# Optimization experiments

Measured on AMD Instinct MI355X. Metric: run time of the kernel, lower is better.

The kernel has to match this reference:

```python
import jax, jax.numpy as jnp
import numpy as np

VOCAB = 32000
D_MODEL = 768
D_FF = 3072
N_LAYERS = 12
SEQ = 2048
BATCH = 8
EPS = 1e-5  # torch LayerNorm default


def _layernorm(x, g, b):
    mu = jnp.mean(x, axis=-1, keepdims=True)
    var = jnp.mean(jnp.square(x - mu), axis=-1, keepdims=True)
    return (x - mu) * jax.lax.rsqrt(var + EPS) * g + b


def setup_inputs() -> dict:
    key = jax.random.key(0)
    ks = jax.random.split(key, 12)
    tokens = jax.random.randint(ks[0], (BATCH, SEQ), 0, VOCAB)
    embed = jax.random.normal(ks[1], (VOCAB, D_MODEL), dtype=jnp.float32) * 0.02
    ln1_g = jnp.ones((N_LAYERS, D_MODEL), dtype=jnp.float32)
    ln1_b = jnp.zeros((N_LAYERS, D_MODEL), dtype=jnp.float32)
    ln2_g = jnp.ones((N_LAYERS, D_MODEL), dtype=jnp.float32)
    ln2_b = jnp.zeros((N_LAYERS, D_MODEL), dtype=jnp.float32)
    W1 = jax.random.normal(ks[2], (N_LAYERS, D_MODEL, D_FF), dtype=jnp.float32) * (1.0 / np.sqrt(D_MODEL))
    b1 = jnp.zeros((N_LAYERS, D_FF), dtype=jnp.float32)
    W2 = jax.random.normal(ks[3], (N_LAYERS, D_FF, D_MODEL), dtype=jnp.float32) * (1.0 / np.sqrt(D_FF))
    b2 = jnp.zeros((N_LAYERS, D_MODEL), dtype=jnp.float32)
    Wout = jax.random.normal(ks[4], (D_MODEL, VOCAB), dtype=jnp.float32) * (1.0 / np.sqrt(D_MODEL))
    bout = jnp.zeros((VOCAB,), dtype=jnp.float32)
    return {"tokens": tokens, "embed": embed, "ln1_g": ln1_g, "ln1_b": ln1_b,
            "ln2_g": ln2_g, "ln2_b": ln2_b, "W1": W1, "b1": b1, "W2": W2, "b2": b2,
            "Wout": Wout, "bout": bout}


def reference(tokens, embed, ln1_g, ln1_b, ln2_g, ln2_b, W1, b1, W2, b2, Wout, bout):
    # embedding lookup; embed_size == d_model so projection is Identity.
    x = embed[tokens]  # [B, S, D]
    # dropout is inference-mode identity
    for l in range(N_LAYERS):
        res = x
        h = _layernorm(x, ln1_g[l], ln1_b[l])
        h = jnp.fft.fft2(h, axes=(-2, -1)).real  # token mixing, keep real part
        x = h + res
        res = x
        h = _layernorm(x, ln2_g[l], ln2_b[l])
        h = jax.nn.gelu(jnp.einsum('bsd,df->bsf', h, W1[l]) + b1[l], approximate=False)
        h = jnp.einsum('bsf,fd->bsd', h, W2[l]) + b2[l]
        x = h + res
    # predict from last position
    return jnp.einsum('bd,dv->bv', x[:, -1, :], Wout) + bout
```

## Files before the change

kernel.cpp:

```cpp
#include <hip/hip_runtime.h>
#include <hip/hip_bf16.h>

typedef unsigned short u16;
typedef unsigned long long u64;
typedef __attribute__((ext_vector_type(8))) __bf16 bf16x8;
typedef __attribute__((ext_vector_type(4))) float f32x4;
typedef __attribute__((ext_vector_type(4))) unsigned short u16x4;

#define BB 8
#define SS 2048
#define DD 768
#define DFF 3072
#define NL 12
#define ROWS (BB*SS)
#define VOC 32000

__device__ __forceinline__ u16 f2bf(float f){
  union { float f; unsigned u; } v; v.f = f;
  unsigned u = v.u;
  u += 0x7FFF + ((u >> 16) & 1);
  return (u16)(u >> 16);
}
__device__ __forceinline__ float bf2f(u16 b){
  union { unsigned u; float f; } v; v.u = ((unsigned)b) << 16; return v.f;
}

__global__ void k_embed(const int* __restrict__ tok, const float4* __restrict__ emb,
                        float4* __restrict__ x){
  int i = blockIdx.x*256 + threadIdx.x;
  if (i >= ROWS*192) return;
  int row = i/192, c = i - row*192;
  x[i] = emb[(long)tok[row]*192 + c];
}

__global__ void k_dftD(u16* __restrict__ out){
  int i = blockIdx.x*256 + threadIdx.x;
  if (i >= 1536*768) return;
  int n = i/768, k = i - n*768;
  int nn = (n < 768) ? n : n - 768;
  int m = (nn*k) % 768;
  float a = 2.0f*(float)m/768.0f;
  out[i] = f2bf((n < 768) ? cospif(a) : sinpif(a));
}

__global__ void k_dftS2(u16* __restrict__ out){
  int i = blockIdx.x*256 + threadIdx.x;
  if (i >= 2048*2048) return;
  int t = i >> 11, slot = i & 2047;
  int ss = (slot <= 1024) ? slot : slot - 1024;
  int m = (t*ss) & 2047;
  float a = (float)m * (1.0f/1024.0f);
  out[i] = f2bf((slot <= 1024) ? cospif(a) : -sinpif(a));
}

template<bool RES>
__global__ void k_ln1_fold(float* __restrict__ x, const u16* __restrict__ t4,
                           const float* __restrict__ bias,
                           const float* __restrict__ g, const float* __restrict__ b,
                           u16* __restrict__ hp, u16* __restrict__ hm){
  int gid = blockIdx.x*4 + (threadIdx.x >> 6);
  if (gid >= 8*1025) return;
  int bb = gid/1025, t = gid - bb*1025;
  int u = (2048 - t) & 2047;
  long rt = (long)bb*2048 + t, ru = (long)bb*2048 + u;
  int lane = threadIdx.x & 63;
  float vt[12], vu[12];
  #pragma unroll
  for (int j = 0; j < 12; j++){
    int e = lane + j*64;
    float a0 = x[rt*DD + e], a1 = x[ru*DD + e];
    if (RES){
      float bv = bias[e];
      a0 += bf2f(t4[rt*DD + e]) + bv;
      a1 += bf2f(t4[ru*DD + e]) + bv;
    }
    vt[j] = a0; vu[j] = a1;
  }
  float s0 = 0.f, s1 = 0.f;
  #pragma unroll
  for (int j = 0; j < 12; j++){ s0 += vt[j]; s1 += vu[j]; }
  #pragma unroll
  for (int o = 32; o > 0; o >>= 1){ s0 += __shfl_xor(s0, o); s1 += __shfl_xor(s1, o); }
  float mu0 = s0*(1.0f/768.0f), mu1 = s1*(1.0f/768.0f);
  float q0 = 0.f, q1 = 0.f;
  #pragma unroll
  for (int j = 0; j < 12; j++){ float d0 = vt[j]-mu0, d1 = vu[j]-mu1; q0 += d0*d0; q1 += d1*d1; }
  #pragma unroll
  for (int o = 32; o > 0; o >>= 1){ q0 += __shfl_xor(q0, o); q1 += __shfl_xor(q1, o); }
  float r0 = rsqrtf(q0*(1.0f/768.0f) + 1e-5f);
  float r1 = rsqrtf(q1*(1.0f/768.0f) + 1e-5f);
  const bool single = (t == 0) || (t == 1024);
  u16* hpr = hp + ((long)bb*1280 + t)*DD;
  u16* hmr = hm + ((long)bb*1024 + t)*DD;
  #pragma unroll
  for (int j = 0; j < 12; j++){
    int e = lane + j*64;
    if (RES){ x[rt*DD + e] = vt[j]; x[ru*DD + e] = vu[j]; }
    float ht = (vt[j]-mu0)*r0*g[e] + b[e];
    float hu = (vu[j]-mu1)*r1*g[e] + b[e];
    hpr[e] = f2bf(single ? ht : ht + hu);
    if (!single) hmr[e] = f2bf(ht - hu);
  }
}

__global__ void k_ln2_fuse(float* __restrict__ x, const u16* __restrict__ t2,
                           const float* __restrict__ g, const float* __restrict__ b,
                           u16* __restrict__ h, int rmul, int radd, int nrows){
  int gid = blockIdx.x*4 + (threadIdx.x >> 6);
  if (gid >= nrows) return;
  long row = (long)gid*rmul + radd;
  int lane = threadIdx.x & 63;
  float v[12];
  float s = 0.f;
  #pragma unroll
  for (int j = 0; j < 12; j++){
    int e = lane + j*64;
    long ix = row*DD + e;
    float a = x[ix] + bf2f(t2[ix]);
    v[j] = a; s += a;
  }
  #pragma unroll
  for (int o = 32; o > 0; o >>= 1) s += __shfl_xor(s, o);
  float mu = s * (1.0f/768.0f);
  float q = 0.f;
  #pragma unroll
  for (int j = 0; j < 12; j++){ float d = v[j]-mu; q += d*d; }
  #pragma unroll
  for (int o = 32; o > 0; o >>= 1) q += __shfl_xor(q, o);
  float rs = rsqrtf(q * (1.0f/768.0f) + 1e-5f);
  #pragma unroll
  for (int j = 0; j < 12; j++){
    int e = lane + j*64;
    x[row*DD + e] = v[j];
    h[row*DD + e] = f2bf((v[j]-mu)*rs*g[e] + b[e]);
  }
}

__global__ void k_transpose_cvt(const float* __restrict__ src, u16* __restrict__ dst,
                                int R, int C){
  __shared__ float t[32][33];
  int bx = blockIdx.x*32, by = blockIdx.y*32;
  int tx = threadIdx.x, ty = threadIdx.y;
  #pragma unroll
  for (int i = 0; i < 4; i++) t[ty+i*8][tx] = src[(long)(by+ty+i*8)*C + bx+tx];
  __syncthreads();
  #pragma unroll
  for (int i = 0; i < 4; i++) dst[(long)(bx+ty+i*8)*R + by+tx] = f2bf(t[tx][ty+i*8]);
}

#define EPI_ADDX 1
#define EPI_GELU 2
#define EPI_OUTB 3

#define MFMA_Q(H, G, BF) do { \
  __builtin_amdgcn_s_setprio(1); \
  _Pragma("unroll") \
  for (int mm = 0; mm < 4; ++mm) \
    _Pragma("unroll") \
    for (int nn = 0; nn < 2; ++nn) \
      _Pragma("unroll") \
      for (int ks2 = 0; ks2 < 2; ++ks2) \
        acc[((H)<<2)+mm][((G)<<1)+nn] = __builtin_amdgcn_mfma_f32_16x16x32_bf16( \
            aF[mm][ks2], BF[nn][ks2], acc[((H)<<2)+mm][((G)<<1)+nn], 0, 0, 0); \
  __builtin_amdgcn_s_setprio(0); \
} while(0)

#define GEMM_CORE_BODY \
  f32x4 acc[8][4] = {}; \
  bf16x8 aF[4][2], b0F[2][2], b1F[2][2]; \
  auto stage = [&](int tile){ \
    if (tile >= NT) return; \
    _Pragma("unroll") \
    for (int hh = 0; hh < 4; ++hh){ \
      const int isB   = ((hh + 1) >> 1) & 1; \
      const int rhalf = ((hh >> 1) & 1) << 7; \
      const u16* src = isB ? Bb : Ab; \
      const int rb = (isB ? bn : bm) + rhalf + sRow; \
      const u16* s0 = src + (long)rb * K + (tile << 6) + sCol; \
      u16* d0 = &lds[tile & 1][isB][rhalf + (wave << 3)][0]; \
      __builtin_amdgcn_global_load_lds((__attribute__((address_space(1))) void*)(s0), \
                                       (__attribute__((address_space(3))) void*)(d0), 16, 0, 0); \
      __builtin_amdgcn_global_load_lds((__attribute__((address_space(1))) void*)(s0 + ((long)K << 6)), \
                                       (__attribute__((address_space(3))) void*)(d0 + 64*64), 16, 0, 0); \
    } \
  }; \
  auto readA = [&](int c, int H){ \
    const u16* base = &lds[c][0][(H << 7) + (wm << 6)][0]; \
    _Pragma("unroll") \
    for (int mm = 0; mm < 4; ++mm) \
      _Pragma("unroll") \
      for (int ks2 = 0; ks2 < 2; ++ks2) \
        aF[mm][ks2] = *(const bf16x8*)&base[((mm<<4) + fr)*64 + (((ks2<<5) + fks8) ^ swz)]; \
  }; \
  auto readB = [&](int c, int G, bf16x8 (&bF)[2][2]){ \
    const u16* base = &lds[c][1][(G << 7) + (wn << 5)][0]; \
    _Pragma("unroll") \
    for (int nn = 0; nn < 2; ++nn) \
      _Pragma("unroll") \
      for (int ks2 = 0; ks2 < 2; ++ks2) \
        bF[nn][ks2] = *(const bf16x8*)&base[((nn<<4) + fr)*64 + (((ks2<<5) + fks8) ^ swz)]; \
  }; \
  stage(0); \
  __syncthreads(); \
  for (int T = 0; T < NT; ++T){ \
    stage(T + 1); \
    int c = T & 1; \
    readA(c, 0); readB(c, 0, b0F); \
    MFMA_Q(0, 0, b0F); \
    readB(c, 1, b1F); \
    MFMA_Q(0, 1, b1F); \
    readA(c, 1); \
    MFMA_Q(1, 1, b1F); \
    MFMA_Q(1, 0, b0F); \
    __syncthreads(); \
  }

template<int EPI>
__global__ __launch_bounds__(512, 2)
void k_gemm256(const u16* __restrict__ A, const u16* __restrict__ BT,
               int Nt, int N, int K, int NT, long aBS, long btBS, int rowOffPerZ,
               int mMul, int mAdd,
               float* __restrict__ X, const float* __restrict__ bias,
               u16* __restrict__ OUT){
  __shared__ __align__(16) u16 lds[2][2][256][64];
  const int tid  = threadIdx.x;
  const int wave = tid >> 6, lane = tid & 63;
  const int wm = wave >> 2, wn = wave & 3;

  const int bz = blockIdx.z;
  const u16* Ab = A + (long)bz*aBS;
  const u16* Bb = BT + (long)bz*btBS;
  const int rowOff = bz*rowOffPerZ;

  const int nwg = gridDim.x;
  const int id  = blockIdx.x;
  const int sw  = ((nwg & 7) == 0) ? ((id & 7) * (nwg >> 3) + (id >> 3)) : id;
  const int bn = (sw % Nt) << 8;
  const int bm = ((sw / Nt) * mMul + mAdd) << 8;

  const int fr   = lane & 15;
  const int fks8 = (lane >> 4) << 3;
  const int swz  = (fr & 7) << 3;
  const int sRow = (wave << 3) + (lane >> 3);
  const int sCol = ((lane & 7) ^ ((lane >> 3) & 7)) << 3;

  GEMM_CORE_BODY

  const int er = (lane >> 4) << 2, ec = lane & 15;
  #pragma unroll
  for (int mi = 0; mi < 8; ++mi){
    int row = bm + ((mi >> 2) << 7) + (wm << 6) + ((mi & 3) << 4) + er;
    #pragma unroll
    for (int ni = 0; ni < 4; ++ni){
      int col = bn + ((ni >> 1) << 7) + (wn << 5) + ((ni & 1) << 4) + ec;
      f32x4 v = acc[mi][ni];
      if constexpr (EPI == EPI_ADDX){
        float bv = bias ? bias[col] : 0.0f;
        #pragma unroll
        for (int r = 0; r < 4; r++)
          X[(long)(rowOff + row + r)*N + col] += v[r] + bv;
      } else if constexpr (EPI == EPI_OUTB){
        #pragma unroll
        for (int r = 0; r < 4; r++)
          OUT[(long)(rowOff + row + r)*N + col] = f2bf(v[r]);
      } else {
        float bv = bias[col];
        #pragma unroll
        for (int r = 0; r < 4; r++){
          float tt = v[r] + bv;
          OUT[(long)(row + r)*N + col] = f2bf(0.5f*tt*(1.0f + erff(tt*0.70710678118654752f)));
        }
      }
    }
  }
}

__global__ __launch_bounds__(512, 2)
void k_gemm1(const u16* __restrict__ hp, const u16* __restrict__ hm,
             const u16* __restrict__ dftD, u16* __restrict__ Ff){
  __shared__ __align__(16) u16 lds[2][2][256][64];
  const int tid  = threadIdx.x;
  const int wave = tid >> 6, lane = tid & 63;
  const int wm = wave >> 2, wn = wave & 3;

  const int K = 768, NT = 12;
  const int nwg = gridDim.x;
  const int id  = blockIdx.x;
  int sw  = (id & 7) * (nwg >> 3) + (id >> 3);
  const bool plus = (sw < 120);
  const u16* Ab;
  const u16* Bb;
  if (plus){ Ab = hp; Bb = dftD; }
  else     { sw -= 120; Ab = hm; Bb = dftD + 768*768; }
  const int bn = (sw % 3) << 8;
  const int bm = (sw / 3) << 8;

  const int fr   = lane & 15;
  const int fks8 = (lane >> 4) << 3;
  const int swz  = (fr & 7) << 3;
  const int sRow = (wave << 3) + (lane >> 3);
  const int sCol = ((lane & 7) ^ ((lane >> 3) & 7)) << 3;

  GEMM_CORE_BODY

  const int er = (lane >> 4) << 2, ec = lane & 15;
  #pragma unroll
  for (int mi = 0; mi < 8; ++mi){
    int row = bm + ((mi >> 2) << 7) + (wm << 6) + ((mi & 3) << 4) + er;
    #pragma unroll
    for (int ni = 0; ni < 4; ++ni){
      int col = bn + ((ni >> 1) << 7) + (wn << 5) + ((ni & 1) << 4) + ec;
      f32x4 v = acc[mi][ni];
      u16x4 pk;
      #pragma unroll
      for (int r = 0; r < 4; r++) pk[r] = f2bf(v[r]);
      if (plus){
        int b = row / 1280, t = row - b*1280;
        u16* dst = Ff + ((long)(b*768 + col))*2048 + t;
        if (t <= 1020)      *(u16x4*)dst = pk;
        else if (t == 1024) dst[0] = pk[0];
      } else {
        int b = row >> 10, t = row & 1023;
        u16* dst = Ff + ((long)(b*768 + col))*2048 + 1024 + t;
        if (t == 0){ dst[1] = pk[1]; dst[2] = pk[2]; dst[3] = pk[3]; }
        else        *(u16x4*)dst = pk;
      }
    }
  }
}

__global__ void k_logits(const float* __restrict__ x, const float* __restrict__ Wout,
                         const float* __restrict__ bout, float* __restrict__ out){
  __shared__ float xl[8][768];
  int tid = threadIdx.x;
  for (int i = tid; i < 8*768; i += 256){
    int b = i/768, d = i - b*768;
    xl[b][d] = x[((long)(b*2048 + 2047))*768 + d];
  }
  __syncthreads();
  int v = blockIdx.x*256 + tid;
  float acc[8];
  float bv = bout[v];
  #pragma unroll
  for (int b = 0; b < 8; b++) acc[b] = bv;
  for (int d = 0; d < 768; d++){
    float w = Wout[(long)d*VOC + v];
    #pragma unroll
    for (int b = 0; b < 8; b++) acc[b] += xl[b][d]*w;
  }
  #pragma unroll
  for (int b = 0; b < 8; b++) out[(long)b*VOC + v] = acc[b];
}

extern "C" void kernel_launch(void* const* d_in, const int* in_sizes, int n_in,
                              void* d_out, int out_size, void* d_ws, size_t ws_size,
                              hipStream_t stream){
  const int*   tokens = (const int*)d_in[0];
  const float* embed  = (const float*)d_in[1];
  const float* ln1_g  = (const float*)d_in[2];
  const float* ln1_b  = (const float*)d_in[3];
  const float* ln2_g  = (const float*)d_in[4];
  const float* ln2_b  = (const float*)d_in[5];
  const float* W1     = (const float*)d_in[6];
  const float* b1     = (const float*)d_in[7];
  const float* W2     = (const float*)d_in[8];
  const float* b2     = (const float*)d_in[9];
  const float* Wout   = (const float*)d_in[10];
  const float* bout   = (const float*)d_in[11];
  float* out = (float*)d_out;

  char* p = (char*)d_ws;
  size_t off = 0;
  auto alloc = [&](size_t bytes)->char*{
    char* r = p + off; off += (bytes + 255) & ~(size_t)255; return r;
  };
  float* x    = (float*)alloc((size_t)ROWS*DD*4);
  u16*   h    = (u16*)  alloc((size_t)ROWS*DD*2);
  u16*  gbuf  = (u16*)  alloc((size_t)ROWS*DFF*2);
  u16*  tmpO  = (u16*)  alloc((size_t)ROWS*DD*2);
  u16*  dftD  = (u16*)  alloc((size_t)1536*768*2);
  u16*  dftS2 = (u16*)  alloc((size_t)2048*2048*2);
  u16*  w1t   = (u16*)  alloc((size_t)DFF*DD*2);
  u16*  w2t   = (u16*)  alloc((size_t)DD*DFF*2);
  if (off > ws_size) return;
  u16* hp = gbuf;
  u16* hm = gbuf + (size_t)8*1280*768;
  u16* Ff = hm   + (size_t)8*1024*768;

  k_dftD<<<(1536*768+255)/256, 256, 0, stream>>>(dftD);
  k_dftS2<<<(2048*2048+255)/256, 256, 0, stream>>>(dftS2);
  k_embed<<<(ROWS*192+255)/256, 256, 0, stream>>>(tokens, (const float4*)embed, (float4*)x);

  for (int l = 0; l < NL; l++){
    const bool last = (l == NL-1);
    if (l == 0)
      k_ln1_fold<false><<<2050, 256, 0, stream>>>(x, nullptr, nullptr,
          ln1_g + l*DD, ln1_b + l*DD, hp, hm);
    else
      k_ln1_fold<true><<<2050, 256, 0, stream>>>(x, tmpO, b2 + (l-1)*DD,
          ln1_g + l*DD, ln1_b + l*DD, hp, hm);
    k_gemm1<<<216, 512, 0, stream>>>(hp, hm, dftD, Ff);
    if (!last)
      k_gemm256<EPI_OUTB><<<dim3(24, 1, 8), 512, 0, stream>>>(
          dftS2, Ff, 3, 768, 2048, 32, 0, (long)768*2048, 2048, 1, 0,
          nullptr, nullptr, tmpO);
    else
      k_gemm256<EPI_OUTB><<<dim3(3, 1, 8), 512, 0, stream>>>(
          dftS2, Ff, 3, 768, 2048, 32, 0, (long)768*2048, 2048, 1, 7,
          nullptr, nullptr, tmpO);
    if (!last)
      k_ln2_fuse<<<4096, 256, 0, stream>>>(x, tmpO,
          ln2_g + l*DD, ln2_b + l*DD, h, 1, 0, 16384);
    else
      k_ln2_fuse<<<2, 256, 0, stream>>>(x, tmpO,
          ln2_g + l*DD, ln2_b + l*DD, h, 2048, 2047, 8);
    k_transpose_cvt<<<dim3(DFF/32, DD/32), dim3(32,8), 0, stream>>>(
        W1 + (long)l*DD*DFF, w1t, DD, DFF);
    k_transpose_cvt<<<dim3(DD/32, DFF/32), dim3(32,8), 0, stream>>>(
        W2 + (long)l*DFF*DD, w2t, DFF, DD);
    if (!last)
      k_gemm256<EPI_GELU><<<768, 512, 0, stream>>>(
          h, w1t, 12, 3072, 768, 12, 0, 0, 0, 1, 0,
          nullptr, b1 + l*DFF, gbuf);
    else
      k_gemm256<EPI_GELU><<<96, 512, 0, stream>>>(
          h, w1t, 12, 3072, 768, 12, 0, 0, 0, 8, 7,
          nullptr, b1 + l*DFF, gbuf);
    if (!last)
      k_gemm256<EPI_OUTB><<<dim3(192, 1, 1), 512, 0, stream>>>(
          gbuf, w2t, 3, 768, 3072, 48, 0, 0, 0, 1, 0,
          nullptr, nullptr, tmpO);
    else
      k_gemm256<EPI_ADDX><<<dim3(24, 1, 1), 512, 0, stream>>>(
          gbuf, w2t, 3, 768, 3072, 48, 0, 0, 0, 8, 7,
          x, b2 + l*DD, nullptr);
  }
  k_logits<<<VOC/256, 256, 0, stream>>>(x, Wout, bout, out);
}
```

Baseline: 4.021 ms.

## Store residual stream in bf16 and merge the two weight transposes into one launch

The fp32 residual buffer x becomes bf16 across the embed, both layernorm kernels, the GEMM add epilogue and the logits kernel, which halves residual read/write traffic in the memory-bound layernorm passes. The two per-layer weight transpose launches are merged into one launch that uses blockIdx.z to pick W1 or W2. The cost is accumulated rounding error in the residual over 12 layers, which could threaten tolerance.

After: 3.861 ms, median of 2. 1.04x faster.

```diff
diff --git a/kernel.cpp b/kernel.cpp
--- a/kernel.cpp
+++ b/kernel.cpp
@@ -26,11 +26,13 @@
 }
 
 __global__ void k_embed(const int* __restrict__ tok, const float4* __restrict__ emb,
-                        float4* __restrict__ x){
+                        u16* __restrict__ x){
   int i = blockIdx.x*256 + threadIdx.x;
   if (i >= ROWS*192) return;
   int row = i/192, c = i - row*192;
-  x[i] = emb[(long)tok[row]*192 + c];
+  float4 v = emb[(long)tok[row]*192 + c];
+  u16x4 o; o[0]=f2bf(v.x); o[1]=f2bf(v.y); o[2]=f2bf(v.z); o[3]=f2bf(v.w);
+  *(u16x4*)&x[(long)i*4] = o;
 }
 
 __global__ void k_dftD(u16* __restrict__ out){
@@ -54,7 +56,7 @@
 }
 
 template<bool RES>
-__global__ void k_ln1_fold(float* __restrict__ x, const u16* __restrict__ t4,
+__global__ void k_ln1_fold(u16* __restrict__ x, const u16* __restrict__ t4,
                            const float* __restrict__ bias,
                            const float* __restrict__ g, const float* __restrict__ b,
                            u16* __restrict__ hp, u16* __restrict__ hm){
@@ -68,7 +70,7 @@
   #pragma unroll
   for (int j = 0; j < 12; j++){
     int e = lane + j*64;
-    float a0 = x[rt*DD + e], a1 = x[ru*DD + e];
+    float a0 = bf2f(x[rt*DD + e]), a1 = bf2f(x[ru*DD + e]);
     if (RES){
       float bv = bias[e];
       a0 += bf2f(t4[rt*DD + e]) + bv;
@@ -95,7 +97,7 @@
   #pragma unroll
   for (int j = 0; j < 12; j++){
     int e = lane + j*64;
-    if (RES){ x[rt*DD + e] = vt[j]; x[ru*DD + e] = vu[j]; }
+    if (RES){ x[rt*DD + e] = f2bf(vt[j]); x[ru*DD + e] = f2bf(vu[j]); }
     float ht = (vt[j]-mu0)*r0*g[e] + b[e];
     float hu = (vu[j]-mu1)*r1*g[e] + b[e];
     hpr[e] = f2bf(single ? ht : ht + hu);
@@ -103,7 +105,7 @@
   }
 }
 
-__global__ void k_ln2_fuse(float* __restrict__ x, const u16* __restrict__ t2,
+__global__ void k_ln2_fuse(u16* __restrict__ x, const u16* __restrict__ t2,
                            const float* __restrict__ g, const float* __restrict__ b,
                            u16* __restrict__ h, int rmul, int radd, int nrows){
   int gid = blockIdx.x*4 + (threadIdx.x >> 6);
@@ -116,7 +118,7 @@
   for (int j = 0; j < 12; j++){
     int e = lane + j*64;
     long ix = row*DD + e;
-    float a = x[ix] + bf2f(t2[ix]);
+    float a = bf2f(x[ix]) + bf2f(t2[ix]);
     v[j] = a; s += a;
   }
   #pragma unroll
@@ -131,15 +133,17 @@
   #pragma unroll
   for (int j = 0; j < 12; j++){
     int e = lane + j*64;
-    x[row*DD + e] = v[j];
+    x[row*DD + e] = f2bf(v[j]);
     h[row*DD + e] = f2bf((v[j]-mu)*rs*g[e] + b[e]);
   }
 }
 
-__global__ void k_transpose_cvt(const float* __restrict__ src, u16* __restrict__ dst,
-                                int R, int C){
+__global__ void k_transpose2(const float* __restrict__ W1, const float* __restrict__ W2,
+                             u16* __restrict__ w1t, u16* __restrict__ w2t){
   __shared__ float t[32][33];
-  int bx = blockIdx.x*32, by = blockIdx.y*32;
+  const float* src; u16* dst; int R, C, bx, by;
+  if (blockIdx.z == 0){ src = W1; dst = w1t; R = DD;  C = DFF; bx = blockIdx.x*32; by = blockIdx.y*32; }
+  else                { src = W2; dst = w2t; R = DFF; C = DD;  bx = blockIdx.y*32; by = blockIdx.x*32; }
   int tx = threadIdx.x, ty = threadIdx.y;
   #pragma unroll
   for (int i = 0; i < 4; i++) t[ty+i*8][tx] = src[(long)(by+ty+i*8)*C + bx+tx];
@@ -148,7 +152,7 @@
   for (int i = 0; i < 4; i++) dst[(long)(bx+ty+i*8)*R + by+tx] = f2bf(t[tx][ty+i*8]);
 }
 
-#define EPI_ADDX 1
+#define EPI_ADDB 1
 #define EPI_GELU 2
 #define EPI_OUTB 3
 
@@ -220,7 +224,7 @@
 void k_gemm256(const u16* __restrict__ A, const u16* __restrict__ BT,
                int Nt, int N, int K, int NT, long aBS, long btBS, int rowOffPerZ,
                int mMul, int mAdd,
-               float* __restrict__ X, const float* __restrict__ bias,
+               u16* __restrict__ X, const float* __restrict__ bias,
                u16* __restrict__ OUT){
   __shared__ __align__(16) u16 lds[2][2][256][64];
   const int tid  = threadIdx.x;
@@ -254,11 +258,13 @@
     for (int ni = 0; ni < 4; ++ni){
       int col = bn + ((ni >> 1) << 7) + (wn << 5) + ((ni & 1) << 4) + ec;
       f32x4 v = acc[mi][ni];
-      if constexpr (EPI == EPI_ADDX){
+      if constexpr (EPI == EPI_ADDB){
         float bv = bias ? bias[col] : 0.0f;
         #pragma unroll
-        for (int r = 0; r < 4; r++)
-          X[(long)(rowOff + row + r)*N + col] += v[r] + bv;
+        for (int r = 0; r < 4; r++){
+          long ix = (long)(rowOff + row + r)*N + col;
+          X[ix] = f2bf(bf2f(X[ix]) + v[r] + bv);
+        }
       } else if constexpr (EPI == EPI_OUTB){
         #pragma unroll
         for (int r = 0; r < 4; r++)
@@ -329,13 +335,13 @@
   }
 }
 
-__global__ void k_logits(const float* __restrict__ x, const float* __restrict__ Wout,
+__global__ void k_logits(const u16* __restrict__ x, const float* __restrict__ Wout,
                          const float* __restrict__ bout, float* __restrict__ out){
   __shared__ float xl[8][768];
   int tid = threadIdx.x;
   for (int i = tid; i < 8*768; i += 256){
     int b = i/768, d = i - b*768;
-    xl[b][d] = x[((long)(b*2048 + 2047))*768 + d];
+    xl[b][d] = bf2f(x[((long)(b*2048 + 2047))*768 + d]);
   }
   __syncthreads();
   int v = blockIdx.x*256 + tid;
@@ -374,7 +380,7 @@
   auto alloc = [&](size_t bytes)->char*{
     char* r = p + off; off += (bytes + 255) & ~(size_t)255; return r;
   };
-  float* x    = (float*)alloc((size_t)ROWS*DD*4);
+  u16*   x    = (u16*)  alloc((size_t)ROWS*DD*2);
   u16*   h    = (u16*)  alloc((size_t)ROWS*DD*2);
   u16*  gbuf  = (u16*)  alloc((size_t)ROWS*DFF*2);
   u16*  tmpO  = (u16*)  alloc((size_t)ROWS*DD*2);
@@ -389,7 +395,7 @@
 
   k_dftD<<<(1536*768+255)/256, 256, 0, stream>>>(dftD);
   k_dftS2<<<(2048*2048+255)/256, 256, 0, stream>>>(dftS2);
-  k_embed<<<(ROWS*192+255)/256, 256, 0, stream>>>(tokens, (const float4*)embed, (float4*)x);
+  k_embed<<<(ROWS*192+255)/256, 256, 0, stream>>>(tokens, (const float4*)embed, x);
 
   for (int l = 0; l < NL; l++){
     const bool last = (l == NL-1);
@@ -414,10 +420,8 @@
     else
       k_ln2_fuse<<<2, 256, 0, stream>>>(x, tmpO,
           ln2_g + l*DD, ln2_b + l*DD, h, 2048, 2047, 8);
-    k_transpose_cvt<<<dim3(DFF/32, DD/32), dim3(32,8), 0, stream>>>(
-        W1 + (long)l*DD*DFF, w1t, DD, DFF);
-    k_transpose_cvt<<<dim3(DD/32, DFF/32), dim3(32,8), 0, stream>>>(
-        W2 + (long)l*DFF*DD, w2t, DFF, DD);
+    k_transpose2<<<dim3(96, 24, 2), dim3(32,8), 0, stream>>>(
+        W1 + (long)l*DD*DFF, W2 + (long)l*DFF*DD, w1t, w2t);
     if (!last)
       k_gemm256<EPI_GELU><<<768, 512, 0, stream>>>(
           h, w1t, 12, 3072, 768, 12, 0, 0, 0, 1, 0,
@@ -431,7 +435,7 @@
           gbuf, w2t, 3, 768, 3072, 48, 0, 0, 0, 1, 0,
           nullptr, nullptr, tmpO);
     else
-      k_gemm256<EPI_ADDX><<<dim3(24, 1, 1), 512, 0, stream>>>(
+      k_gemm256<EPI_ADDB><<<dim3(24, 1, 1), 512, 0, stream>>>(
           gbuf, w2t, 3, 768, 3072, 48, 0, 0, 0, 8, 7,
           x, b2 + l*DD, nullptr);
   }
```
